# Performance work log

Measured on AMD Instinct MI355X. Metric: run time of the kernel, lower is better.

Reference implementation:

```python
import jax, jax.numpy as jnp
import numpy as np

TAU = 0.07
EPS_NORM = 1e-12
EPS_DEN = 1e-8


def setup_inputs() -> dict:
    key = jax.random.key(0)
    k1, k2, k3, k4 = jax.random.split(key, 4)
    B, C, H, W = 2, 128, 64, 64
    return {
        "input": jax.random.normal(k1, (B, C, H, W), dtype=jnp.float32),
        "target": jax.random.normal(k2, (B, C, H, W), dtype=jnp.float32),
        "input_seg": jax.random.randint(k3, (B, H, W), 0, 4, dtype=jnp.int64 if jax.config.jax_enable_x64 else jnp.int32),
        "target_seg": jax.random.randint(k4, (B, H, W), 0, 4, dtype=jnp.int64 if jax.config.jax_enable_x64 else jnp.int32),
    }


def _flatten_normalize(x):
    # (B, C, H, W) -> (B*H*W, C), L2-normalized rows (torch F.normalize semantics)
    B, C = x.shape[0], x.shape[1]
    x = jnp.moveaxis(x, 1, -1).reshape(-1, C)
    norm = jnp.linalg.norm(x, axis=-1, keepdims=True)
    return x / jnp.maximum(norm, EPS_NORM)


def reference(input, target, input_seg, target_seg):
    ni = _flatten_normalize(input)    # (N, C)
    nt = _flatten_normalize(target)   # (N, C)
    pi = input_seg.reshape(-1)        # (N,)
    pt = target_seg.reshape(-1)       # (N,)

    # sim[a, b] = cos(target[a], input[b]); rows already unit-norm so dot == cosine
    sim = jnp.einsum("ac,bc->ab", nt, ni)
    sim_exp = jnp.exp(sim / TAU)

    # diff[a, b] = 1 if pred_input[b] != pred_target[a]
    diff = (pi[None, :] != pt[:, None]).astype(jnp.float32)

    nominator = jnp.sum((1.0 - diff) * sim_exp, axis=0)          # (N,) positives per input pixel
    denominator = jnp.sum(diff * sim_exp, axis=0) + nominator    # (N,) all pairs
    loss = -jnp.log(nominator / (denominator + EPS_DEN)).mean()
    return loss
```

## Files before the change

### kernel.cpp

```cpp
#include <hip/hip_runtime.h>

#define N_PIX 8192
#define C_DIM 128
#define TAU_INV_LOG2E 20.609929155556622f
#define EPS_DEN 1e-8f
#define NT_TILES 68
#define NT_ROWS (NT_TILES * 128)
#define FAKE_ROWS (NT_ROWS - N_PIX)

typedef unsigned short u16;
typedef __attribute__((ext_vector_type(8))) short short8;
typedef __attribute__((ext_vector_type(4))) float f32x4;

__device__ __forceinline__ u16 f2bf(float f) {
    unsigned u = __float_as_uint(f);
    return (u16)((u + 0x7fffu + ((u >> 16) & 1u)) >> 16);
}

__global__ __launch_bounds__(256) void norm_write_k(const float* __restrict__ input,
                                                    const float* __restrict__ target,
                                                    const int* __restrict__ tseg,
                                                    int* __restrict__ meta,
                                                    u16* __restrict__ ni_bf,
                                                    u16* __restrict__ nt_sorted,
                                                    float* __restrict__ den,
                                                    float* __restrict__ nom) {
    __shared__ float tile[128][65];
    __shared__ float sscale[64];
    __shared__ int sdest[64];
    __shared__ int chunkcnt[256][4];
    __shared__ int pfx[256][4];
    __shared__ int tot[4];

    int arr = blockIdx.z;
    int bb = blockIdx.y;
    int hw0 = blockIdx.x * 64;
    int bi = bb * 64 + blockIdx.x;
    const float* src = (arr ? target : input) + bb * (C_DIM * 4096);
    int t = threadIdx.x;
    int lane = t & 63, w = t >> 6;
    int tq = w, tl = lane;

    if (arr == 0) {
        if (t < 64) den[bi * 64 + t] = 0.f;
        else if (t < 128) nom[bi * 64 + (t - 64)] = 0.f;
    }

#pragma unroll
    for (int i = 0; i < 32; ++i) {
        int c = i * 4 + tq;
        tile[c][tl] = src[c * 4096 + hw0 + tl];
    }

    int ps[5];
    int padc[4];
    if (arr) {
        int v[8][4];
        int c0 = 0, c1 = 0, c2 = 0, c3 = 0;
        const int4* ts4 = (const int4*)tseg;
#pragma unroll
        for (int j = 0; j < 8; ++j) {
            int4 x = ts4[t * 8 + j];
            c0 += (x.x == 0) + (x.y == 0) + (x.z == 0) + (x.w == 0);
            c1 += (x.x == 1) + (x.y == 1) + (x.z == 1) + (x.w == 1);
            c2 += (x.x == 2) + (x.y == 2) + (x.z == 2) + (x.w == 2);
            c3 += (x.x == 3) + (x.y == 3) + (x.z == 3) + (x.w == 3);
        }
        (void)v;
        chunkcnt[t][0] = c0; chunkcnt[t][1] = c1; chunkcnt[t][2] = c2; chunkcnt[t][3] = c3;
    }
    __syncthreads();

    if (arr) {
        int c = w;
        int vv[4];
#pragma unroll
        for (int j = 0; j < 4; ++j) vv[j] = chunkcnt[lane * 4 + j][c];
        int s = vv[0] + vv[1] + vv[2] + vv[3];
        int si = s;
#pragma unroll
        for (int off = 1; off < 64; off <<= 1) {
            int y = __shfl_up(si, off);
            if (lane >= off) si += y;
        }
        int run = si - s;
#pragma unroll
        for (int j = 0; j < 4; ++j) { pfx[lane * 4 + j][c] = run; run += vv[j]; }
        if (lane == 63) tot[c] = si;
    }
    __syncthreads();

    if (arr) {
        ps[0] = 0;
#pragma unroll
        for (int c = 0; c < 4; ++c) {
            int tc = tot[c];
            int padded = (tc + 127) & ~127;
            ps[c + 1] = ps[c] + padded;
            padc[c] = padded - tc;
        }
        if (blockIdx.x == 0 && bb == 0) {
            if (t < 4) meta[12 + t] = padc[t];
            if (t < NT_TILES) {
                int row = t * 128, cl = 4;
#pragma unroll
                for (int c = 0; c < 4; ++c)
                    if (row >= ps[c] && row < ps[c + 1]) cl = c;
                meta[16 + t] = cl;
            }
        }
        if (t < 64) {
            int g = bi + (t >> 4) * 128;
            int gg = g, c;
            for (c = 0; c < 4; ++c) { if (gg < padc[c]) break; gg -= padc[c]; }
            int row = (c < 4) ? (ps[c + 1] - padc[c] + gg) : (ps[4] + gg);
            short8 z = {};
            *(short8*)(nt_sorted + (long)row * C_DIM + (t & 15) * 8) = z;
        }
    }

    int p = t >> 2, sub = t & 3;
    float ss = 0.f;
#pragma unroll
    for (int i = 0; i < 32; ++i) {
        float vv = tile[sub * 32 + i][p];
        ss += vv * vv;
    }
    ss += __shfl_xor(ss, 1);
    ss += __shfl_xor(ss, 2);
    if (sub == 0) {
        float sc = 1.0f / fmaxf(sqrtf(ss), 1e-12f);
        int n = bb * 4096 + hw0 + p;
        int dst_row;
        if (arr) {
            sc *= TAU_INV_LOG2E;
            int c = tseg[n];
            int chunk = n >> 5, pos = n & 31;
            int r = 0;
            for (int j = 0; j < pos; ++j) r += (tseg[chunk * 32 + j] == c);
            dst_row = ps[c] + pfx[chunk][c] + r;
        } else {
            dst_row = n;
        }
        sscale[p] = sc;
        sdest[p] = dst_row;
    }
    __syncthreads();

    u16* dst = arr ? nt_sorted : ni_bf;
#pragma unroll
    for (int i = 0; i < 4; ++i) {
        int idx = t + i * 256;
        int px = idx >> 4, kc = idx & 15;
        float sc = sscale[px];
        long drow = sdest[px];
        short8 o;
#pragma unroll
        for (int j = 0; j < 8; ++j)
            o[j] = (short)f2bf(tile[kc * 8 + j][px] * sc);
        *(short8*)(dst + drow * C_DIM + kc * 8) = o;
    }
}

__global__ __launch_bounds__(256, 2) void main_k(const u16* __restrict__ ni,
                                                 const u16* __restrict__ nt,
                                                 const int* __restrict__ piseg,
                                                 const int* __restrict__ meta,
                                                 float* __restrict__ den,
                                                 float* __restrict__ nom) {
    __shared__ __align__(16) u16 sA[128 * 136];

    int bcb = blockIdx.x & 63;
    int as  = blockIdx.x >> 6;
    int t0  = as * 8 + (as < 4 ? as : 4);
    int ntl = 8 + (as < 4 ? 1 : 0);
    int bcol0 = bcb * 128;
    int tid = threadIdx.x;
    int lane = tid & 63;
    int wave = tid >> 6;
    int wr = wave >> 1, wc = wave & 1;
    int l15 = lane & 15, q = lane >> 4;
    const int* tcls = meta + 16;

    short8 bfrag[4][4];
    int pil[4];
#pragma unroll
    for (int ct = 0; ct < 4; ++ct) {
        int brow = bcol0 + wc * 64 + ct * 16 + l15;
        pil[ct] = piseg[brow];
        const u16* bp = ni + brow * C_DIM + q * 8;
#pragma unroll
        for (int kc = 0; kc < 4; ++kc)
            bfrag[ct][kc] = *(const short8*)(bp + kc * 32);
    }

    float den_l[4] = {0.f, 0.f, 0.f, 0.f};
    float nom_l[4] = {0.f, 0.f, 0.f, 0.f};

    for (int it = 0; it < ntl; ++it) {
        int tile = t0 + it;
        int a0 = tile * 128;
        __syncthreads();
        {
            const uint4* gsrc = (const uint4*)(nt + (long)a0 * C_DIM);
#pragma unroll
            for (int i = 0; i < 8; ++i) {
                int idx = tid + i * 256;
                int r = idx >> 4, ch = idx & 15;
                *(uint4*)(&sA[r * 136 + ch * 8]) = gsrc[idx];
            }
        }
        __syncthreads();

        f32x4 acc[4][4] = {};
#pragma unroll
        for (int kc = 0; kc < 4; ++kc) {
            short8 af[4];
#pragma unroll
            for (int rt = 0; rt < 4; ++rt) {
                int ar = wr * 64 + rt * 16 + l15;
                af[rt] = *(const short8*)(&sA[ar * 136 + kc * 32 + q * 8]);
            }
#pragma unroll
            for (int rt = 0; rt < 4; ++rt)
#pragma unroll
                for (int ct = 0; ct < 4; ++ct)
                    acc[rt][ct] = __builtin_amdgcn_mfma_f32_16x16x32_bf16(
                        af[rt], bfrag[ct][kc], acc[rt][ct], 0, 0, 0);
        }

        int tc = tcls[tile];
        float td[4] = {0.f, 0.f, 0.f, 0.f};
#pragma unroll
        for (int rt = 0; rt < 4; ++rt)
#pragma unroll
            for (int ct = 0; ct < 4; ++ct) {
                f32x4 v = acc[rt][ct];
                float e0 = __builtin_amdgcn_exp2f(v[0]);
                float e1 = __builtin_amdgcn_exp2f(v[1]);
                float e2 = __builtin_amdgcn_exp2f(v[2]);
                float e3 = __builtin_amdgcn_exp2f(v[3]);
                td[ct] += (e0 + e1) + (e2 + e3);
            }
#pragma unroll
        for (int ct = 0; ct < 4; ++ct) {
            den_l[ct] += td[ct];
            nom_l[ct] += (tc == pil[ct]) ? td[ct] : 0.f;
        }
    }

#pragma unroll
    for (int ct = 0; ct < 4; ++ct) {
        float d = den_l[ct], nm = nom_l[ct];
        d += __shfl_xor(d, 16); d += __shfl_xor(d, 32);
        nm += __shfl_xor(nm, 16); nm += __shfl_xor(nm, 32);
        if (lane < 16) {
            int b = bcol0 + wc * 64 + ct * 16 + lane;
            atomicAdd(&den[b], d);
            atomicAdd(&nom[b], nm);
        }
    }
}

__global__ __launch_bounds__(1024) void loss_k(const float* __restrict__ den,
                                               const float* __restrict__ nom,
                                               const int* __restrict__ piseg,
                                               const int* __restrict__ meta,
                                               float* __restrict__ out) {
    int t = threadIdx.x;
    float padcf[4];
#pragma unroll
    for (int c = 0; c < 4; ++c) padcf[c] = (float)meta[12 + c];
    int base = t * 8;
    float s = 0.f;
#pragma unroll
    for (int h = 0; h < 2; ++h) {
        float4 d4 = *(const float4*)(den + base + h * 4);
        float4 n4 = *(const float4*)(nom + base + h * 4);
        int4  p4 = *(const int4*)(piseg + base + h * 4);
        float dd[4] = {d4.x, d4.y, d4.z, d4.w};
        float nn[4] = {n4.x, n4.y, n4.z, n4.w};
        int   pp[4] = {p4.x, p4.y, p4.z, p4.w};
#pragma unroll
        for (int j = 0; j < 4; ++j) {
            float nm = nn[j] - padcf[pp[j]];
            float d = dd[j] - (float)FAKE_ROWS;
            s -= __logf(nm / (d + EPS_DEN));
        }
    }
#pragma unroll
    for (int off = 32; off > 0; off >>= 1) s += __shfl_down(s, off);
    __shared__ float part[16];
    int wave = t >> 6;
    if ((t & 63) == 0) part[wave] = s;
    __syncthreads();
    if (t == 0) {
        float acc = 0.f;
#pragma unroll
        for (int i = 0; i < 16; ++i) acc += part[i];
        out[0] = acc * (1.0f / N_PIX);
    }
}

extern "C" void kernel_launch(void* const* d_in, const int* in_sizes, int n_in,
                              void* d_out, int out_size, void* d_ws, size_t ws_size,
                              hipStream_t stream) {
    const float* input  = (const float*)d_in[0];
    const float* target = (const float*)d_in[1];
    const int*   iseg   = (const int*)d_in[2];
    const int*   tseg   = (const int*)d_in[3];
    float* out = (float*)d_out;

    char* ws = (char*)d_ws;
    u16* ni_bf     = (u16*)(ws);
    u16* nt_sorted = (u16*)(ws + 0x200000);
    float* den     = (float*)(ws + 0x420000);
    float* nom     = (float*)(ws + 0x428000);
    int* meta      = (int*)(ws + 0x430000);

    norm_write_k<<<dim3(64, 2, 2), 256, 0, stream>>>(input, target, tseg, meta,
                                                     ni_bf, nt_sorted, den, nom);
    main_k<<<512, 256, 0, stream>>>(ni_bf, nt_sorted, iseg, meta, den, nom);
    loss_k<<<1, 1024, 0, stream>>>(den, nom, iseg, meta, out);
}
```

Baseline: 94.46 us.

## Fuse normalize, similarity, and loss kernels into one cooperative grid-synced kernel

Merges the three kernels into a single cooperative launch of 512 blocks, with grid.sync between the normalize/sort phase, the MFMA similarity phase and the final loss reduction. The phase-1 work is split over 512 blocks of 32 pixels instead of 256 blocks of 64, the LDS tile drops padding in favour of an XOR swizzle, and the phases share LDS through a union. If the cooperative launch fails, a two-kernel fallback runs, using a last-block atomic counter for the loss. This is meant to remove launch gaps and the single-block loss kernel, at the cost of grid-wide barrier overhead and requiring all 512 blocks to be co-resident.

```diff
diff --git a/kernel.cpp b/kernel.cpp
--- a/kernel.cpp
+++ b/kernel.cpp
@@ -1,4 +1,5 @@
 #include <hip/hip_runtime.h>
+#include <hip/hip_cooperative_groups.h>
 
 #define N_PIX 8192
 #define C_DIM 128
@@ -17,45 +18,51 @@
     return (u16)((u + 0x7fffu + ((u >> 16) & 1u)) >> 16);
 }
 
-__global__ __launch_bounds__(256) void norm_write_k(const float* __restrict__ input,
-                                                    const float* __restrict__ target,
-                                                    const int* __restrict__ tseg,
-                                                    int* __restrict__ meta,
-                                                    u16* __restrict__ ni_bf,
-                                                    u16* __restrict__ nt_sorted,
-                                                    float* __restrict__ den,
-                                                    float* __restrict__ nom) {
-    __shared__ float tile[128][65];
-    __shared__ float sscale[64];
-    __shared__ int sdest[64];
-    __shared__ int chunkcnt[256][4];
-    __shared__ int pfx[256][4];
-    __shared__ int tot[4];
-
-    int arr = blockIdx.z;
-    int bb = blockIdx.y;
-    int hw0 = blockIdx.x * 64;
-    int bi = bb * 64 + blockIdx.x;
+struct P1 {
+    float tile[128][33];
+    float sscale[32];
+    int sdest[32];
+    int chunkcnt[256][4];
+    int pfx[256][4];
+    int tot[4];
+};
+struct P2 { u16 sA[128 * 128]; };
+struct P3 { float part[4]; };
+union SMem { P1 p1; P2 p2; P3 p3; };
+
+
+__device__ __forceinline__ void phase1(SMem& sm, int bid, int t,
+                                       const float* __restrict__ input,
+                                       const float* __restrict__ target,
+                                       const int* __restrict__ tseg,
+                                       int* __restrict__ meta,
+                                       u16* __restrict__ ni_bf,
+                                       u16* __restrict__ nt_sorted,
+                                       float* __restrict__ den,
+                                       float* __restrict__ nom) {
+    int lane = t & 63, w = t >> 6;
+    int arr = bid >> 8;
+    int u = bid & 255;
+    int bb = u >> 7;
+    int hw0 = (u & 127) * 32;
     const float* src = (arr ? target : input) + bb * (C_DIM * 4096);
-    int t = threadIdx.x;
-    int lane = t & 63, w = t >> 6;
-    int tq = w, tl = lane;
 
     if (arr == 0) {
-        if (t < 64) den[bi * 64 + t] = 0.f;
-        else if (t < 128) nom[bi * 64 + (t - 64)] = 0.f;
-    }
-
-#pragma unroll
-    for (int i = 0; i < 32; ++i) {
-        int c = i * 4 + tq;
-        tile[c][tl] = src[c * 4096 + hw0 + tl];
-    }
-
-    int ps[5];
-    int padc[4];
+        if (t < 32) den[u * 32 + t] = 0.f;
+        else if (t < 64) nom[u * 32 + (t - 32)] = 0.f;
+        if (bid == 0 && t == 64) meta[8] = 0;
+    }
+
+    int c8 = t >> 5, hwl = t & 31;
+#pragma unroll
+    for (int i = 0; i < 16; ++i) {
+        int c = i * 8 + c8;
+        sm.p1.tile[c][hwl] = src[c * 4096 + hw0 + hwl];
+    }
+
+    int ps[5] = {0, 0, 0, 0, 0};
+    int padc[4] = {0, 0, 0, 0};
     if (arr) {
-        int v[8][4];
         int c0 = 0, c1 = 0, c2 = 0, c3 = 0;
         const int4* ts4 = (const int4*)tseg;
 #pragma unroll
@@ -66,8 +73,8 @@
             c2 += (x.x == 2) + (x.y == 2) + (x.z == 2) + (x.w == 2);
             c3 += (x.x == 3) + (x.y == 3) + (x.z == 3) + (x.w == 3);
         }
-        (void)v;
-        chunkcnt[t][0] = c0; chunkcnt[t][1] = c1; chunkcnt[t][2] = c2; chunkcnt[t][3] = c3;
+        sm.p1.chunkcnt[t][0] = c0; sm.p1.chunkcnt[t][1] = c1;
+        sm.p1.chunkcnt[t][2] = c2; sm.p1.chunkcnt[t][3] = c3;
     }
     __syncthreads();
 
@@ -75,7 +82,7 @@
         int c = w;
         int vv[4];
 #pragma unroll
-        for (int j = 0; j < 4; ++j) vv[j] = chunkcnt[lane * 4 + j][c];
+        for (int j = 0; j < 4; ++j) vv[j] = sm.p1.chunkcnt[lane * 4 + j][c];
         int s = vv[0] + vv[1] + vv[2] + vv[3];
         int si = s;
 #pragma unroll
@@ -85,21 +92,20 @@
         }
         int run = si - s;
 #pragma unroll
-        for (int j = 0; j < 4; ++j) { pfx[lane * 4 + j][c] = run; run += vv[j]; }
-        if (lane == 63) tot[c] = si;
+        for (int j = 0; j < 4; ++j) { sm.p1.pfx[lane * 4 + j][c] = run; run += vv[j]; }
+        if (lane == 63) sm.p1.tot[c] = si;
     }
     __syncthreads();
 
     if (arr) {
-        ps[0] = 0;
 #pragma unroll
         for (int c = 0; c < 4; ++c) {
-            int tc = tot[c];
+            int tc = sm.p1.tot[c];
             int padded = (tc + 127) & ~127;
             ps[c + 1] = ps[c] + padded;
             padc[c] = padded - tc;
         }
-        if (blockIdx.x == 0 && bb == 0) {
+        if (u == 0) {
             if (t < 4) meta[12 + t] = padc[t];
             if (t < NT_TILES) {
                 int row = t * 128, cl = 4;
@@ -109,8 +115,8 @@
                 meta[16 + t] = cl;
             }
         }
-        if (t < 64) {
-            int g = bi + (t >> 4) * 128;
+        if (t < 32) {
+            int g = u * 2 + (t >> 4);
             int gg = g, c;
             for (c = 0; c < 4; ++c) { if (gg < padc[c]) break; gg -= padc[c]; }
             int row = (c < 4) ? (ps[c + 1] - padc[c] + gg) : (ps[4] + gg);
@@ -119,66 +125,64 @@
         }
     }
 
-    int p = t >> 2, sub = t & 3;
+    int p = t >> 3, sub = t & 7;
     float ss = 0.f;
 #pragma unroll
-    for (int i = 0; i < 32; ++i) {
-        float vv = tile[sub * 32 + i][p];
+    for (int i = 0; i < 16; ++i) {
+        float vv = sm.p1.tile[sub * 16 + i][p];
         ss += vv * vv;
     }
     ss += __shfl_xor(ss, 1);
     ss += __shfl_xor(ss, 2);
+    ss += __shfl_xor(ss, 4);
     if (sub == 0) {
         float sc = 1.0f / fmaxf(sqrtf(ss), 1e-12f);
         int n = bb * 4096 + hw0 + p;
         int dst_row;
         if (arr) {
             sc *= TAU_INV_LOG2E;
-            int c = tseg[n];
-            int chunk = n >> 5, pos = n & 31;
+            int cme = tseg[n];
+            const int* tc32 = tseg + (n & ~31);
             int r = 0;
-            for (int j = 0; j < pos; ++j) r += (tseg[chunk * 32 + j] == c);
-            dst_row = ps[c] + pfx[chunk][c] + r;
+            for (int j = 0; j < p; ++j) r += (tc32[j] == cme);
+            dst_row = ps[cme] + sm.p1.pfx[n >> 5][cme] + r;
         } else {
             dst_row = n;
         }
-        sscale[p] = sc;
-        sdest[p] = dst_row;
+        sm.p1.sscale[p] = sc;
+        sm.p1.sdest[p] = dst_row;
     }
     __syncthreads();
 
     u16* dst = arr ? nt_sorted : ni_bf;
 #pragma unroll
-    for (int i = 0; i < 4; ++i) {
+    for (int i = 0; i < 2; ++i) {
         int idx = t + i * 256;
         int px = idx >> 4, kc = idx & 15;
-        float sc = sscale[px];
-        long drow = sdest[px];
+        float sc = sm.p1.sscale[px];
+        long drow = sm.p1.sdest[px];
         short8 o;
 #pragma unroll
         for (int j = 0; j < 8; ++j)
-            o[j] = (short)f2bf(tile[kc * 8 + j][px] * sc);
+            o[j] = (short)f2bf(sm.p1.tile[kc * 8 + j][px] * sc);
         *(short8*)(dst + drow * C_DIM + kc * 8) = o;
     }
 }
 
-__global__ __launch_bounds__(256, 2) void main_k(const u16* __restrict__ ni,
-                                                 const u16* __restrict__ nt,
-                                                 const int* __restrict__ piseg,
-                                                 const int* __restrict__ meta,
-                                                 float* __restrict__ den,
-                                                 float* __restrict__ nom) {
-    __shared__ __align__(16) u16 sA[128 * 136];
-
-    int bcb = blockIdx.x & 63;
-    int as  = blockIdx.x >> 6;
+__device__ __forceinline__ void phase2(SMem& sm, int bid, int t,
+                                       const u16* __restrict__ ni,
+                                       const u16* __restrict__ nt,
+                                       const int* __restrict__ piseg,
+                                       const int* __restrict__ meta,
+                                       float* __restrict__ den,
+                                       float* __restrict__ nom) {
+    int lane = t & 63, w = t >> 6;
+    int bcb = bid & 63;
+    int as  = bid >> 6;
     int t0  = as * 8 + (as < 4 ? as : 4);
     int ntl = 8 + (as < 4 ? 1 : 0);
     int bcol0 = bcb * 128;
-    int tid = threadIdx.x;
-    int lane = tid & 63;
-    int wave = tid >> 6;
-    int wr = wave >> 1, wc = wave & 1;
+    int wr = w >> 1, wc = w & 1;
     int l15 = lane & 15, q = lane >> 4;
     const int* tcls = meta + 16;
 
@@ -205,9 +209,10 @@
             const uint4* gsrc = (const uint4*)(nt + (long)a0 * C_DIM);
 #pragma unroll
             for (int i = 0; i < 8; ++i) {
-                int idx = tid + i * 256;
+                int idx = t + i * 256;
                 int r = idx >> 4, ch = idx & 15;
-                *(uint4*)(&sA[r * 136 + ch * 8]) = gsrc[idx];
+                int sw = ch ^ (r & 15);
+                *(uint4*)(&sm.p2.sA[r * 128 + sw * 8]) = gsrc[idx];
             }
         }
         __syncthreads();
@@ -219,7 +224,8 @@
 #pragma unroll
             for (int rt = 0; rt < 4; ++rt) {
                 int ar = wr * 64 + rt * 16 + l15;
-                af[rt] = *(const short8*)(&sA[ar * 136 + kc * 32 + q * 8]);
+                int sw = (kc * 4 + q) ^ l15;
+                af[rt] = *(const short8*)(&sm.p2.sA[ar * 128 + sw * 8]);
             }
 #pragma unroll
             for (int rt = 0; rt < 4; ++rt)
@@ -262,19 +268,19 @@
     }
 }
 
-__global__ __launch_bounds__(1024) void loss_k(const float* __restrict__ den,
-                                               const float* __restrict__ nom,
-                                               const int* __restrict__ piseg,
-                                               const int* __restrict__ meta,
-                                               float* __restrict__ out) {
-    int t = threadIdx.x;
+__device__ __forceinline__ void phase3(SMem& sm, int t,
+                                       const float* __restrict__ den,
+                                       const float* __restrict__ nom,
+                                       const int* __restrict__ piseg,
+                                       const int* __restrict__ meta,
+                                       float* __restrict__ out) {
     float padcf[4];
 #pragma unroll
     for (int c = 0; c < 4; ++c) padcf[c] = (float)meta[12 + c];
-    int base = t * 8;
+    int base = t * 32;
     float s = 0.f;
 #pragma unroll
-    for (int h = 0; h < 2; ++h) {
+    for (int h = 0; h < 8; ++h) {
         float4 d4 = *(const float4*)(den + base + h * 4);
         float4 n4 = *(const float4*)(nom + base + h * 4);
         int4  p4 = *(const int4*)(piseg + base + h * 4);
@@ -290,15 +296,68 @@
     }
 #pragma unroll
     for (int off = 32; off > 0; off >>= 1) s += __shfl_down(s, off);
-    __shared__ float part[16];
-    int wave = t >> 6;
-    if ((t & 63) == 0) part[wave] = s;
+    if ((t & 63) == 0) sm.p3.part[t >> 6] = s;
+    __syncthreads();
+    if (t == 0)
+        out[0] = (sm.p3.part[0] + sm.p3.part[1] + sm.p3.part[2] + sm.p3.part[3])
+                 * (1.0f / N_PIX);
+}
+
+__global__ __launch_bounds__(256, 2) void fused_k(const float* __restrict__ input,
+                                                  const float* __restrict__ target,
+                                                  const int* __restrict__ tseg,
+                                                  const int* __restrict__ piseg,
+                                                  int* __restrict__ meta,
+                                                  u16* __restrict__ ni_bf,
+                                                  u16* __restrict__ nt_sorted,
+                                                  float* __restrict__ den,
+                                                  float* __restrict__ nom,
+                                                  float* __restrict__ out) {
+    cooperative_groups::grid_group grid = cooperative_groups::this_grid();
+    __shared__ __align__(16) SMem sm;
+    int bid = blockIdx.x, t = threadIdx.x;
+    phase1(sm, bid, t, input, target, tseg, meta, ni_bf, nt_sorted, den, nom);
+    __threadfence();
+    grid.sync();
+    phase2(sm, bid, t, ni_bf, nt_sorted, piseg, meta, den, nom);
+    __threadfence();
+    grid.sync();
+    if (bid == 0) phase3(sm, t, den, nom, piseg, meta, out);
+}
+
+__global__ __launch_bounds__(256) void p1_k(const float* __restrict__ input,
+                                            const float* __restrict__ target,
+                                            const int* __restrict__ tseg,
+                                            int* __restrict__ meta,
+                                            u16* __restrict__ ni_bf,
+                                            u16* __restrict__ nt_sorted,
+                                            float* __restrict__ den,
+                                            float* __restrict__ nom) {
+    __shared__ __align__(16) SMem sm;
+    phase1(sm, blockIdx.x, threadIdx.x, input, target, tseg, meta, ni_bf, nt_sorted, den, nom);
+}
+
+__global__ __launch_bounds__(256, 2) void main_loss_k(const u16* __restrict__ ni,
+                                                      const u16* __restrict__ nt,
+                                                      const int* __restrict__ piseg,
+                                                      int* __restrict__ meta,
+                                                      float* __restrict__ den,
+                                                      float* __restrict__ nom,
+                                                      float* __restrict__ out) {
+    __shared__ __align__(16) SMem sm;
+    __shared__ int is_last;
+    int t = threadIdx.x;
+    phase2(sm, blockIdx.x, t, ni, nt, piseg, meta, den, nom);
+    __threadfence();
     __syncthreads();
     if (t == 0) {
-        float acc = 0.f;
-#pragma unroll
-        for (int i = 0; i < 16; ++i) acc += part[i];
-        out[0] = acc * (1.0f / N_PIX);
+        int tk = atomicAdd(&meta[8], 1);
+        is_last = (tk == 511);
+    }
+    __syncthreads();
+    if (is_last) {
+        __threadfence();
+        phase3(sm, t, den, nom, piseg, meta, out);
     }
 }
 
@@ -318,8 +377,14 @@
     float* nom     = (float*)(ws + 0x428000);
     int* meta      = (int*)(ws + 0x430000);
 
-    norm_write_k<<<dim3(64, 2, 2), 256, 0, stream>>>(input, target, tseg, meta,
-                                                     ni_bf, nt_sorted, den, nom);
-    main_k<<<512, 256, 0, stream>>>(ni_bf, nt_sorted, iseg, meta, den, nom);
-    loss_k<<<1, 1024, 0, stream>>>(den, nom, iseg, meta, out);
-}
+    void* kargs[] = {(void*)&input, (void*)&target, (void*)&tseg, (void*)&iseg,
+                     (void*)&meta, (void*)&ni_bf, (void*)&nt_sorted,
+                     (void*)&den, (void*)&nom, (void*)&out};
+    hipError_t e = hipLaunchCooperativeKernel((void*)fused_k, dim3(512), dim3(256),
+                                              kargs, 0, stream);
+    if (e != hipSuccess) {
+        (void)hipGetLastError();
+        p1_k<<<512, 256, 0, stream>>>(input, target, tseg, meta, ni_bf, nt_sorted, den, nom);
+        main_loss_k<<<512, 256, 0, stream>>>(ni_bf, nt_sorted, iseg, meta, den, nom, out);
+    }
+}
```

Result: slower. 285.8 us (+202.5%).
